# Kernel tuning notes

Hardware: AMD Instinct MI355X
Metric: run time of the kernel (lower is better)

## Reference

```python
import jax, jax.numpy as jnp
import numpy as np


def setup_inputs() -> dict:
    key = jax.random.key(0)
    k1, k2 = jax.random.split(key)
    B, M, N, D = 8, 2048, 2048, 1024
    x = jax.random.normal(k1, (B, M, D), dtype=jnp.float32)
    y = jax.random.normal(k2, (B, N, D), dtype=jnp.float32)
    return {"x": x, "y": y}


def reference(x, y):
    # scores e[b,m,n] = <x[b,m], y[b,n]>   (K.batch_dot(x, y, axes=2))
    e = jnp.einsum('bmd,bnd->bmn', x, y)
    # stable softmax over last axis (the exp/max/sum sequence in the original)
    p = jax.nn.softmax(e, axis=-1)
    # K.batch_dot(z, x, axes=1): contract axis 1 (m) of both -> [B, n, d]; V = x
    out = jnp.einsum('bmn,bmd->bnd', p, x)
    return out
```

## Files before the change

### kernel.cpp

```cpp
#include <hip/hip_runtime.h>
#include <hip/hip_bf16.h>
#include <stdint.h>

#define B_ 8
#define M_ 2048
#define N_ 2048
#define D_ 1024

typedef __bf16 bf16x8 __attribute__((ext_vector_type(8)));
typedef float f32x4 __attribute__((ext_vector_type(4)));
typedef uint16_t us4 __attribute__((ext_vector_type(4)));
typedef uint16_t us8 __attribute__((ext_vector_type(8)));

__device__ __forceinline__ uint16_t f2b(float f) {
    uint32_t u = __float_as_uint(f);
    return (uint16_t)((u + 0x7FFFu + ((u >> 16) & 1u)) >> 16);
}
__device__ __forceinline__ float b2f(uint16_t h) {
    return __uint_as_float(((uint32_t)h) << 16);
}

__device__ __forceinline__ void gld16(const uint16_t* g, const uint16_t* l) {
    __builtin_amdgcn_global_load_lds(
        (const __attribute__((address_space(1))) uint32_t*)g,
        (__attribute__((address_space(3))) uint32_t*)l,
        16, 0, 0);
}

__global__ __launch_bounds__(256) void k_split(const float* __restrict__ x,
                                               const float* __restrict__ y,
                                               uint16_t* __restrict__ xh, uint16_t* __restrict__ xl,
                                               uint16_t* __restrict__ yh, uint16_t* __restrict__ yl) {
    const int i = (blockIdx.x * 256 + threadIdx.x) * 4;
    float4 vx = *(const float4*)(x + i);
    float4 vy = *(const float4*)(y + i);
    float fx[4] = {vx.x, vx.y, vx.z, vx.w};
    float fy[4] = {vy.x, vy.y, vy.z, vy.w};
    us4 hx, lx, hy, ly;
#pragma unroll
    for (int k = 0; k < 4; ++k) {
        uint16_t h = f2b(fx[k]);
        hx[k] = h; lx[k] = f2b(fx[k] - b2f(h));
        uint16_t g = f2b(fy[k]);
        hy[k] = g; ly[k] = f2b(fy[k] - b2f(g));
    }
    *(us4*)(xh + i) = hx;
    *(us4*)(xl + i) = lx;
    *(us4*)(yh + i) = hy;
    *(us4*)(yl + i) = ly;
}

__global__ __launch_bounds__(512, 2) void k_gemm1(const uint16_t* __restrict__ xh,
                                                  const uint16_t* __restrict__ xl,
                                                  const uint16_t* __restrict__ yh,
                                                  const uint16_t* __restrict__ yl,
                                                  float* __restrict__ e,
                                                  float* __restrict__ pmax,
                                                  float* __restrict__ psum) {
    const int b = blockIdx.z;
    const int m0 = blockIdx.x * 256;
    const int n0 = blockIdx.y * 256;
    __shared__ __align__(16) uint16_t lds[65536];

    const int tid = threadIdx.x;
    const int lane = tid & 63;
    const int wid = tid >> 6;
    const int wm = (wid >> 2) * 128;
    const int wn = (wid & 3) * 64;
    const int quad = lane >> 4;
    const int r16 = lane & 15;
    const int swz8 = (quad ^ ((r16 >> 1) & 3)) * 8;

    const int base_row = wid * 16 + (lane >> 2);
    const int gd8 = ((lane & 3) ^ ((lane >> 3) & 3)) * 8;
    const uint16_t* gp[4];
    gp[0] = xh + ((size_t)b * M_ + m0 + base_row) * D_ + gd8;
    gp[1] = xl + ((size_t)b * M_ + m0 + base_row) * D_ + gd8;
    gp[2] = yh + ((size_t)b * N_ + n0 + base_row) * D_ + gd8;
    gp[3] = yl + ((size_t)b * N_ + n0 + base_row) * D_ + gd8;
    const int ldsW = wid * 512;

    const int abase = (wm + r16) * 32 + swz8;
    const int bbase = 16384 + (wn + r16) * 32 + swz8;

    f32x4 acc[8][4];
#pragma unroll
    for (int i = 0; i < 8; ++i)
#pragma unroll
        for (int j = 0; j < 4; ++j) acc[i][j] = (f32x4){0.f, 0.f, 0.f, 0.f};

    auto STAGE = [&](int dst, int ktn, int c0, int c1) {
#pragma unroll
        for (int c = c0; c < c1; ++c)
            gld16(gp[c >> 1] + (size_t)(c & 1) * (128 * D_) + ktn * 32,
                  &lds[dst + c * 4096 + ldsW]);
    };

    STAGE(0, 0, 0, 8);

    for (int kt = 0; kt < D_ / 32; ++kt) {
        const int bo = (kt & 1) << 15;
        const int nbo = bo ^ 32768;

        if (kt < D_ / 32 - 1) {
            STAGE(nbo, kt + 1, 0, 4);
            asm volatile("s_waitcnt vmcnt(4)" ::: "memory");
        } else {
            asm volatile("s_waitcnt vmcnt(0)" ::: "memory");
        }
        __builtin_amdgcn_s_barrier();
        __builtin_amdgcn_sched_barrier(0);

        bf16x8 bh[4], bl[4], ah[8], al[8];
#pragma unroll
        for (int j = 0; j < 4; ++j) {
            bh[j] = *(const bf16x8*)&lds[bo + bbase + j * 512];
            bl[j] = *(const bf16x8*)&lds[bo + bbase + 8192 + j * 512];
        }
        auto RDA = [&](int i) {
            ah[i] = *(const bf16x8*)&lds[bo + abase + i * 512];
            al[i] = *(const bf16x8*)&lds[bo + abase + 8192 + i * 512];
        };
        auto MM = [&](int i) {
#pragma unroll
            for (int j = 0; j < 4; ++j) {
                acc[i][j] = __builtin_amdgcn_mfma_f32_16x16x32_bf16(ah[i], bh[j], acc[i][j], 0, 0, 0);
                acc[i][j] = __builtin_amdgcn_mfma_f32_16x16x32_bf16(ah[i], bl[j], acc[i][j], 0, 0, 0);
                acc[i][j] = __builtin_amdgcn_mfma_f32_16x16x32_bf16(al[i], bh[j], acc[i][j], 0, 0, 0);
            }
        };

        RDA(0); RDA(1); RDA(2); RDA(3);
        __builtin_amdgcn_s_setprio(1); MM(0); MM(1); __builtin_amdgcn_s_setprio(0);
        __builtin_amdgcn_s_barrier(); __builtin_amdgcn_sched_barrier(0);
        if (kt < D_ / 32 - 1) STAGE(nbo, kt + 1, 4, 8);
        RDA(4); RDA(5);
        __builtin_amdgcn_s_setprio(1); MM(2); MM(3); __builtin_amdgcn_s_setprio(0);
        __builtin_amdgcn_s_barrier(); __builtin_amdgcn_sched_barrier(0);
        RDA(6); RDA(7);
        __builtin_amdgcn_s_setprio(1); MM(4); MM(5); __builtin_amdgcn_s_setprio(0);
        __builtin_amdgcn_s_barrier(); __builtin_amdgcn_sched_barrier(0);
        __builtin_amdgcn_s_setprio(1); MM(6); MM(7); __builtin_amdgcn_s_setprio(0);
        __builtin_amdgcn_s_barrier(); __builtin_amdgcn_sched_barrier(0);
    }

    float* eb = e + (size_t)b * M_ * N_;
    const int grows = (int)gridDim.z * M_;
    const int growbase = b * M_ + m0 + wm;
    const int nb = (n0 + wn) >> 6;
    float* pm = pmax + (size_t)nb * grows + growbase;
    float* ps = psum + (size_t)nb * grows + growbase;

#pragma unroll
    for (int i = 0; i < 8; ++i) {
#pragma unroll
        for (int r = 0; r < 4; ++r) {
            const float v0 = acc[i][0][r], v1 = acc[i][1][r];
            const float v2 = acc[i][2][r], v3 = acc[i][3][r];
            float mrow = fmaxf(fmaxf(v0, v1), fmaxf(v2, v3));
#pragma unroll
            for (int s = 1; s < 16; s <<= 1) mrow = fmaxf(mrow, __shfl_xor(mrow, s, 64));
            float srow = __expf(v0 - mrow) + __expf(v1 - mrow)
                       + __expf(v2 - mrow) + __expf(v3 - mrow);
#pragma unroll
            for (int s = 1; s < 16; s <<= 1) srow += __shfl_xor(srow, s, 64);
            const int lrow = i * 16 + quad * 4 + r;
            if (r16 == 0) { pm[lrow] = mrow; ps[lrow] = srow; }
            const size_t ebase = (size_t)(m0 + wm + lrow) * N_ + n0 + wn + r16;
#pragma unroll
            for (int j = 0; j < 4; ++j) eb[ebase + j * 16] = acc[i][j][r];
        }
    }
}

__global__ __launch_bounds__(256) void k_combine(const float* __restrict__ pmax,
                                                 const float* __restrict__ psum,
                                                 float* __restrict__ mx,
                                                 float* __restrict__ inv, int rows) {
    const int r = blockIdx.x * 256 + threadIdx.x;
    float m = -3.4e38f;
#pragma unroll
    for (int nb = 0; nb < 32; ++nb) m = fmaxf(m, pmax[(size_t)nb * rows + r]);
    float s = 0.f;
#pragma unroll
    for (int nb = 0; nb < 32; ++nb)
        s += psum[(size_t)nb * rows + r] * __expf(pmax[(size_t)nb * rows + r] - m);
    mx[r] = m;
    inv[r] = 1.0f / s;
}

__global__ __launch_bounds__(256) void k_texp(const float* __restrict__ e,
                                              const float* __restrict__ mx,
                                              const float* __restrict__ inv,
                                              uint16_t* __restrict__ pT) {
    const int b = blockIdx.z, m0 = blockIdx.x * 64, n0 = blockIdx.y * 64;
    __shared__ float tile[64 * 65];
    const int t = threadIdx.x;
    const float* eb = e + (size_t)b * M_ * N_;
#pragma unroll
    for (int q = 0; q < 4; ++q) {
        const int row = q * 16 + (t >> 4);
        const int c4 = (t & 15) * 4;
        float4 v = *(const float4*)&eb[(size_t)(m0 + row) * N_ + n0 + c4];
        const float mv = mx[b * M_ + m0 + row];
        const float iv = inv[b * M_ + m0 + row];
        tile[row * 65 + c4 + 0] = __expf(v.x - mv) * iv;
        tile[row * 65 + c4 + 1] = __expf(v.y - mv) * iv;
        tile[row * 65 + c4 + 2] = __expf(v.z - mv) * iv;
        tile[row * 65 + c4 + 3] = __expf(v.w - mv) * iv;
    }
    __syncthreads();
    uint16_t* pb = pT + (size_t)b * N_ * M_;
#pragma unroll
    for (int q = 0; q < 2; ++q) {
        const int n = q * 32 + (t >> 3);
        const int mc = (t & 7) * 8;
        us8 o;
#pragma unroll
        for (int k = 0; k < 8; ++k) o[k] = f2b(tile[(mc + k) * 65 + n]);
        *(us8*)&pb[(size_t)(n0 + n) * M_ + m0 + mc] = o;
    }
}

__global__ __launch_bounds__(256) void k_tx(const float* __restrict__ x,
                                            uint16_t* __restrict__ xt) {
    const int b = blockIdx.z, m0 = blockIdx.x * 64, d0 = blockIdx.y * 64;
    __shared__ float tile[64 * 65];
    const int t = threadIdx.x;
    const float* xb = x + (size_t)b * M_ * D_;
#pragma unroll
    for (int q = 0; q < 4; ++q) {
        const int row = q * 16 + (t >> 4);
        const int c4 = (t & 15) * 4;
        float4 v = *(const float4*)&xb[(size_t)(m0 + row) * D_ + d0 + c4];
        tile[row * 65 + c4 + 0] = v.x;
        tile[row * 65 + c4 + 1] = v.y;
        tile[row * 65 + c4 + 2] = v.z;
        tile[row * 65 + c4 + 3] = v.w;
    }
    __syncthreads();
    uint16_t* xtb = xt + (size_t)b * D_ * M_;
#pragma unroll
    for (int q = 0; q < 2; ++q) {
        const int d = q * 32 + (t >> 3);
        const int mc = (t & 7) * 8;
        us8 o;
#pragma unroll
        for (int k = 0; k < 8; ++k) o[k] = f2b(tile[(mc + k) * 65 + d]);
        *(us8*)&xtb[(size_t)(d0 + d) * M_ + m0 + mc] = o;
    }
}

__global__ __launch_bounds__(256) void k_gemm2(const uint16_t* __restrict__ pT,
                                               const uint16_t* __restrict__ xt,
                                               float* __restrict__ out) {
    const int b = blockIdx.z;
    const int n0 = blockIdx.x * 128;
    const int d0 = blockIdx.y * 128;
    __shared__ __align__(16) uint16_t lds[16384];

    const int tid = threadIdx.x;
    const int lane = tid & 63;
    const int wid = tid >> 6;
    const int wn = (wid & 1) * 64;
    const int wd = (wid >> 1) * 64;
    const int quad = lane >> 4;
    const int r16 = lane & 15;

    const uint16_t* srcA = pT + ((size_t)b * N_ + n0) * M_;
    const uint16_t* srcB = xt + ((size_t)b * D_ + d0) * M_;

    f32x4 acc[4][4];
#pragma unroll
    for (int i = 0; i < 4; ++i)
#pragma unroll
        for (int j = 0; j < 4; ++j) acc[i][j] = (f32x4){0.f, 0.f, 0.f, 0.f};

    for (int kt = 0; kt < M_ / 64; ++kt) {
#pragma unroll
        for (int c = 0; c < 8; ++c) {
            const int offbase = c * 2048 + wid * 512;
            const int tile = offbase >> 13;
            const int o = (offbase & 8191) + lane * 8;
            const int row = o >> 6;
            const int gp = (o & 63) >> 3;
            const int gd = gp ^ (row & 7);
            const uint16_t* sp = tile ? srcB : srcA;
            gld16(sp + (size_t)row * M_ + kt * 64 + gd * 8, &lds[offbase]);
        }
        __syncthreads();

#pragma unroll
        for (int h = 0; h < 2; ++h) {
            const int p = (h * 4 + quad) ^ (r16 & 7);
            bf16x8 a[4], bb[4];
#pragma unroll
            for (int i = 0; i < 4; ++i) {
                a[i]  = *(const bf16x8*)&lds[(wn + i * 16 + r16) * 64 + p * 8];
                bb[i] = *(const bf16x8*)&lds[8192 + (wd + i * 16 + r16) * 64 + p * 8];
            }
#pragma unroll
            for (int i = 0; i < 4; ++i)
#pragma unroll
                for (int j = 0; j < 4; ++j)
                    acc[i][j] = __builtin_amdgcn_mfma_f32_16x16x32_bf16(a[i], bb[j], acc[i][j], 0, 0, 0);
        }
        __syncthreads();
    }

    float* ob = out + (size_t)b * N_ * D_;
#pragma unroll
    for (int i = 0; i < 4; ++i) {
        const int rbase = n0 + wn + i * 16 + quad * 4;
#pragma unroll
        for (int j = 0; j < 4; ++j) {
            const int col = d0 + wd + j * 16 + r16;
#pragma unroll
            for (int r = 0; r < 4; ++r)
                ob[(size_t)(rbase + r) * D_ + col] = acc[i][j][r];
        }
    }
}

extern "C" void kernel_launch(void* const* d_in, const int* in_sizes, int n_in,
                              void* d_out, int out_size, void* d_ws, size_t ws_size,
                              hipStream_t stream) {
    const float* x = (const float*)d_in[0];
    const float* y = (const float*)d_in[1];
    float* out = (float*)d_out;
    char* ws = (char*)d_ws;

    const size_t MiB = 1024 * 1024;
    int g = 8;
    while (g > 1 && (size_t)g * 32 * MiB > ws_size) g >>= 1;
    if ((size_t)g * 32 * MiB > ws_size) return;

    const size_t T = (size_t)g * M_ * D_ * 2;
    uint16_t* xh = (uint16_t*)(ws + 0 * T);
    uint16_t* xl = (uint16_t*)(ws + 1 * T);
    uint16_t* yh = (uint16_t*)(ws + 2 * T);
    uint16_t* yl = (uint16_t*)(ws + 3 * T);
    float*    e  = (float*)(ws + 4 * T);
    float*    mx = (float*)(ws);
    float*    inv = mx + (size_t)g * M_;
    uint16_t* xt = xl;
    uint16_t* pT = yh;

    const size_t pelems = (size_t)32 * g * M_;
    float* pmax = (float*)d_out + (size_t)B_ * N_ * D_ - 2 * pelems;
    float* psum = pmax + pelems;

    for (int c0 = 0; c0 < B_; c0 += g) {
        const float* xc = x + (size_t)c0 * M_ * D_;
        const float* yc = y + (size_t)c0 * N_ * D_;
        float* oc = out + (size_t)c0 * N_ * D_;

        hipLaunchKernelGGL(k_split, dim3((g * M_ * D_) / (256 * 4)), dim3(256), 0, stream,
                           xc, yc, xh, xl, yh, yl);
        hipLaunchKernelGGL(k_gemm1, dim3(M_ / 256, N_ / 256, g), dim3(512), 0, stream,
                           xh, xl, yh, yl, e, pmax, psum);
        hipLaunchKernelGGL(k_combine, dim3((g * M_) / 256), dim3(256), 0, stream,
                           pmax, psum, mx, inv, g * M_);
        hipLaunchKernelGGL(k_texp, dim3(M_ / 64, N_ / 64, g), dim3(256), 0, stream,
                           e, mx, inv, pT);
        hipLaunchKernelGGL(k_tx, dim3(M_ / 64, D_ / 64, g), dim3(256), 0, stream, xc, xt);
        hipLaunchKernelGGL(k_gemm2, dim3(N_ / 128, D_ / 128, g), dim3(256), 0, stream,
                           pT, xt, oc);
    }
}
```

Baseline: 507.4 us.

## Restructure split-bf16 GEMM1 as a K-extended GEMM with interleaved staging

The score GEMM no longer issues three MFMAs per k-step over hi/lo pairs. It now treats the computation as one longer K loop of 3×1024 that walks the (xh,yh), (xh,yl) and (xl,yh) segments with 64-wide k tiles. LDS tiles change to 64-column swizzled rows, the A and B buffers are double-buffered on separate schedules, and global-to-LDS loads are spread across four MFMA phases with barriers between them. The aim is fewer register-resident fragments and better overlap of loads with MFMA work, at the cost of more barriers and harder-to-follow buffer indexing.

```diff
diff --git a/kernel.cpp b/kernel.cpp
--- a/kernel.cpp
+++ b/kernel.cpp
@@ -49,6 +49,28 @@
     *(us4*)(yh + i) = hy;
     *(us4*)(yl + i) = ly;
 }
+
+#define BAR1 do { __builtin_amdgcn_sched_barrier(0); __builtin_amdgcn_s_barrier(); \
+                  __builtin_amdgcn_sched_barrier(0); } while (0)
+#define LD8(off) (*(const bf16x8*)&lds[off])
+#define RDA(bo32, q)                                                   \
+    a[0][0] = LD8((bo32) + aoff + ((q)*2) * 1024 + e0);                \
+    a[0][1] = LD8((bo32) + aoff + ((q)*2) * 1024 + e1);                \
+    a[1][0] = LD8((bo32) + aoff + ((q)*2 + 1) * 1024 + e0);            \
+    a[1][1] = LD8((bo32) + aoff + ((q)*2 + 1) * 1024 + e1);
+#define RDB(bo32)                                                      \
+    _Pragma("unroll") for (int j = 0; j < 4; ++j) {                    \
+        bb[j][0] = LD8((bo32) + boff + j * 1024 + e0);                 \
+        bb[j][1] = LD8((bo32) + boff + j * 1024 + e1);                 \
+    }
+#define MFMA16(q)                                                      \
+    __builtin_amdgcn_s_setprio(1);                                     \
+    _Pragma("unroll") for (int kh = 0; kh < 2; ++kh)                   \
+    _Pragma("unroll") for (int ii = 0; ii < 2; ++ii)                   \
+    _Pragma("unroll") for (int j = 0; j < 4; ++j)                      \
+        acc[(q)*2 + ii][j] = __builtin_amdgcn_mfma_f32_16x16x32_bf16(  \
+            a[ii][kh], bb[j][kh], acc[(q)*2 + ii][j], 0, 0, 0);        \
+    __builtin_amdgcn_s_setprio(0);
 
 __global__ __launch_bounds__(512, 2) void k_gemm1(const uint16_t* __restrict__ xh,
                                                   const uint16_t* __restrict__ xl,
@@ -69,19 +91,25 @@
     const int wn = (wid & 3) * 64;
     const int quad = lane >> 4;
     const int r16 = lane & 15;
-    const int swz8 = (quad ^ ((r16 >> 1) & 3)) * 8;
-
-    const int base_row = wid * 16 + (lane >> 2);
-    const int gd8 = ((lane & 3) ^ ((lane >> 3) & 3)) * 8;
-    const uint16_t* gp[4];
-    gp[0] = xh + ((size_t)b * M_ + m0 + base_row) * D_ + gd8;
-    gp[1] = xl + ((size_t)b * M_ + m0 + base_row) * D_ + gd8;
-    gp[2] = yh + ((size_t)b * N_ + n0 + base_row) * D_ + gd8;
-    gp[3] = yl + ((size_t)b * N_ + n0 + base_row) * D_ + gd8;
-    const int ldsW = wid * 512;
-
-    const int abase = (wm + r16) * 32 + swz8;
-    const int bbase = 16384 + (wn + r16) * 32 + swz8;
+    const int rb7 = r16 & 7;
+    const int e0 = (quad ^ rb7) * 8;
+    const int e1 = ((quad + 4) ^ rb7) * 8;
+    const int aoff = (wm + r16) * 64;
+    const int boff = 16384 + (wn + r16) * 64;
+
+    const int srow = tid >> 3;
+    const int gd8 = ((tid & 7) ^ ((tid >> 3) & 7)) * 8;
+
+    auto Ab = [&](int kt) {
+        return (kt < 32 ? xh : xl) + ((size_t)b * M_ + m0) * D_ + (kt & 15) * 64 + gd8;
+    };
+    auto Bb = [&](int kt) {
+        return (((kt >> 4) == 1) ? yl : yh) + ((size_t)b * N_ + n0) * D_ + (kt & 15) * 64 + gd8;
+    };
+    auto SH = [&](int dst, const uint16_t* srcb, int h) {
+        gld16(srcb + (size_t)(h * 128 + srow) * D_, &lds[dst + h * 8192 + wid * 512]);
+        gld16(srcb + (size_t)(h * 128 + 64 + srow) * D_, &lds[dst + h * 8192 + 4096 + wid * 512]);
+    };
 
     f32x4 acc[8][4];
 #pragma unroll
@@ -89,59 +117,57 @@
 #pragma unroll
         for (int j = 0; j < 4; ++j) acc[i][j] = (f32x4){0.f, 0.f, 0.f, 0.f};
 
-    auto STAGE = [&](int dst, int ktn, int c0, int c1) {
-#pragma unroll
-        for (int c = c0; c < c1; ++c)
-            gld16(gp[c >> 1] + (size_t)(c & 1) * (128 * D_) + ktn * 32,
-                  &lds[dst + c * 4096 + ldsW]);
-    };
-
-    STAGE(0, 0, 0, 8);
-
-    for (int kt = 0; kt < D_ / 32; ++kt) {
-        const int bo = (kt & 1) << 15;
-        const int nbo = bo ^ 32768;
-
-        if (kt < D_ / 32 - 1) {
-            STAGE(nbo, kt + 1, 0, 4);
-            asm volatile("s_waitcnt vmcnt(4)" ::: "memory");
-        } else {
-            asm volatile("s_waitcnt vmcnt(0)" ::: "memory");
-        }
-        __builtin_amdgcn_s_barrier();
-        __builtin_amdgcn_sched_barrier(0);
-
-        bf16x8 bh[4], bl[4], ah[8], al[8];
-#pragma unroll
-        for (int j = 0; j < 4; ++j) {
-            bh[j] = *(const bf16x8*)&lds[bo + bbase + j * 512];
-            bl[j] = *(const bf16x8*)&lds[bo + bbase + 8192 + j * 512];
-        }
-        auto RDA = [&](int i) {
-            ah[i] = *(const bf16x8*)&lds[bo + abase + i * 512];
-            al[i] = *(const bf16x8*)&lds[bo + abase + 8192 + i * 512];
-        };
-        auto MM = [&](int i) {
-#pragma unroll
-            for (int j = 0; j < 4; ++j) {
-                acc[i][j] = __builtin_amdgcn_mfma_f32_16x16x32_bf16(ah[i], bh[j], acc[i][j], 0, 0, 0);
-                acc[i][j] = __builtin_amdgcn_mfma_f32_16x16x32_bf16(ah[i], bl[j], acc[i][j], 0, 0, 0);
-                acc[i][j] = __builtin_amdgcn_mfma_f32_16x16x32_bf16(al[i], bh[j], acc[i][j], 0, 0, 0);
-            }
-        };
-
-        RDA(0); RDA(1); RDA(2); RDA(3);
-        __builtin_amdgcn_s_setprio(1); MM(0); MM(1); __builtin_amdgcn_s_setprio(0);
-        __builtin_amdgcn_s_barrier(); __builtin_amdgcn_sched_barrier(0);
-        if (kt < D_ / 32 - 1) STAGE(nbo, kt + 1, 4, 8);
-        RDA(4); RDA(5);
-        __builtin_amdgcn_s_setprio(1); MM(2); MM(3); __builtin_amdgcn_s_setprio(0);
-        __builtin_amdgcn_s_barrier(); __builtin_amdgcn_sched_barrier(0);
-        RDA(6); RDA(7);
-        __builtin_amdgcn_s_setprio(1); MM(4); MM(5); __builtin_amdgcn_s_setprio(0);
-        __builtin_amdgcn_s_barrier(); __builtin_amdgcn_sched_barrier(0);
-        __builtin_amdgcn_s_setprio(1); MM(6); MM(7); __builtin_amdgcn_s_setprio(0);
-        __builtin_amdgcn_s_barrier(); __builtin_amdgcn_sched_barrier(0);
+    bf16x8 a[2][2], bb[4][2];
+
+    SH(0, Ab(0), 0); SH(0, Ab(0), 1);
+    SH(16384, Bb(0), 0); SH(16384, Bb(0), 1);
+    SH(49152, Bb(1), 0); SH(49152, Bb(1), 1);
+    asm volatile("s_waitcnt vmcnt(4)" ::: "memory");
+    __builtin_amdgcn_s_barrier();
+    __builtin_amdgcn_sched_barrier(0);
+
+    for (int t = 0; t < 24; ++t) {
+        const bool s2 = t < 23;
+        const uint16_t* a1p = Ab(2 * t + 1);
+        const uint16_t* a2p = Ab(2 * t + 2);
+        const uint16_t* b2p = Bb(2 * t + 2);
+        const uint16_t* b3p = Bb(2 * t + 3);
+
+        RDB(0); RDA(0, 0);
+        SH(32768, a1p, 0);
+        BAR1; MFMA16(0); BAR1;
+
+        RDA(0, 1);
+        SH(32768, a1p, 1);
+        if (s2) SH(16384, b2p, 0);
+        BAR1; MFMA16(1); BAR1;
+
+        RDA(0, 2);
+        if (s2) SH(16384, b2p, 1);
+        BAR1; MFMA16(2); BAR1;
+
+        RDA(0, 3);
+        BAR1; MFMA16(3);
+        if (s2) { asm volatile("s_waitcnt vmcnt(4)" ::: "memory"); }
+        else    { asm volatile("s_waitcnt vmcnt(0)" ::: "memory"); }
+        BAR1;
+
+        RDB(32768); RDA(32768, 0);
+        if (s2) SH(0, a2p, 0);
+        BAR1; MFMA16(0); BAR1;
+
+        RDA(32768, 1);
+        if (s2) { SH(0, a2p, 1); SH(49152, b3p, 0); }
+        BAR1; MFMA16(1); BAR1;
+
+        RDA(32768, 2);
+        if (s2) SH(49152, b3p, 1);
+        BAR1; MFMA16(2); BAR1;
+
+        RDA(32768, 3);
+        BAR1; MFMA16(3);
+        if (s2) { asm volatile("s_waitcnt vmcnt(4)" ::: "memory"); }
+        BAR1;
     }
 
     float* eb = e + (size_t)b * M_ * N_;
@@ -160,12 +186,12 @@
             float mrow = fmaxf(fmaxf(v0, v1), fmaxf(v2, v3));
 #pragma unroll
             for (int s = 1; s < 16; s <<= 1) mrow = fmaxf(mrow, __shfl_xor(mrow, s, 64));
-            float srow = __expf(v0 - mrow) + __expf(v1 - mrow)
-                       + __expf(v2 - mrow) + __expf(v3 - mrow);
-#pragma unroll
-            for (int s = 1; s < 16; s <<= 1) srow += __shfl_xor(srow, s, 64);
+            float srow_ = __expf(v0 - mrow) + __expf(v1 - mrow)
+                        + __expf(v2 - mrow) + __expf(v3 - mrow);
+#pragma unroll
+            for (int s = 1; s < 16; s <<= 1) srow_ += __shfl_xor(srow_, s, 64);
             const int lrow = i * 16 + quad * 4 + r;
-            if (r16 == 0) { pm[lrow] = mrow; ps[lrow] = srow; }
+            if (r16 == 0) { pm[lrow] = mrow; ps[lrow] = srow_; }
             const size_t ebase = (size_t)(m0 + wm + lrow) * N_ + n0 + wn + r16;
 #pragma unroll
             for (int j = 0; j < 4; ++j) eb[ebase + j * 16] = acc[i][j][r];
@@ -293,17 +319,17 @@
 #pragma unroll
         for (int h = 0; h < 2; ++h) {
             const int p = (h * 4 + quad) ^ (r16 & 7);
-            bf16x8 a[4], bb[4];
+            bf16x8 a[4], bbr[4];
 #pragma unroll
             for (int i = 0; i < 4; ++i) {
-                a[i]  = *(const bf16x8*)&lds[(wn + i * 16 + r16) * 64 + p * 8];
-                bb[i] = *(const bf16x8*)&lds[8192 + (wd + i * 16 + r16) * 64 + p * 8];
+                a[i]   = *(const bf16x8*)&lds[(wn + i * 16 + r16) * 64 + p * 8];
+                bbr[i] = *(const bf16x8*)&lds[8192 + (wd + i * 16 + r16) * 64 + p * 8];
             }
 #pragma unroll
             for (int i = 0; i < 4; ++i)
 #pragma unroll
                 for (int j = 0; j < 4; ++j)
-                    acc[i][j] = __builtin_amdgcn_mfma_f32_16x16x32_bf16(a[i], bb[j], acc[i][j], 0, 0, 0);
+                    acc[i][j] = __builtin_amdgcn_mfma_f32_16x16x32_bf16(a[i], bbr[j], acc[i][j], 0, 0, 0);
         }
         __syncthreads();
     }
```

After: 515.0 us. About the same (+1.5%).

## Software-pipeline LDS fragment reads in gemm1 with ping-pong A registers

Applied to the files above, without the earlier changes.

Restructures the k_gemm1 main loop so the A fragments for the next quarter are read from LDS while MFMAs for the current quarter run, using two ping-pong register sets. The next K-tile's first A and B fragments are prefetched before the loop iteration ends. The number of workgroup barriers per tile drops from five to two, and the global-to-LDS stage is issued as one batch of eight loads. This hides LDS latency behind matrix work and cuts barrier stalls, but it waits on all outstanding global loads (vmcnt(0)) mid-iteration, which may expose global latency, and it raises register pressure. Variable renames elsewhere are cosmetic.

```diff
diff --git a/kernel.cpp b/kernel.cpp
--- a/kernel.cpp
+++ b/kernel.cpp
@@ -49,6 +49,31 @@
     *(us4*)(yh + i) = hy;
     *(us4*)(yl + i) = ly;
 }
+
+#define SBAR0 __builtin_amdgcn_sched_barrier(0)
+#define LD8(off) (*(const bf16x8*)&lds[off])
+#define RDB(bo)                                                        \
+    _Pragma("unroll") for (int j = 0; j < 4; ++j) {                    \
+        bh[j] = LD8((bo) + bbase + j * 512);                           \
+        bl[j] = LD8((bo) + bbase + 8192 + j * 512);                    \
+    }
+#define RDA(H, L, bo, q)                                               \
+    H[0] = LD8((bo) + abase + ((q)*2) * 512);                          \
+    H[1] = LD8((bo) + abase + ((q)*2 + 1) * 512);                      \
+    L[0] = LD8((bo) + abase + 8192 + ((q)*2) * 512);                   \
+    L[1] = LD8((bo) + abase + 8192 + ((q)*2 + 1) * 512);
+#define MMQ(H, L, q)                                                   \
+    __builtin_amdgcn_s_setprio(1);                                     \
+    _Pragma("unroll") for (int ii = 0; ii < 2; ++ii)                   \
+    _Pragma("unroll") for (int j = 0; j < 4; ++j) {                    \
+        acc[(q)*2 + ii][j] = __builtin_amdgcn_mfma_f32_16x16x32_bf16(  \
+            H[ii], bh[j], acc[(q)*2 + ii][j], 0, 0, 0);                \
+        acc[(q)*2 + ii][j] = __builtin_amdgcn_mfma_f32_16x16x32_bf16(  \
+            H[ii], bl[j], acc[(q)*2 + ii][j], 0, 0, 0);                \
+        acc[(q)*2 + ii][j] = __builtin_amdgcn_mfma_f32_16x16x32_bf16(  \
+            L[ii], bh[j], acc[(q)*2 + ii][j], 0, 0, 0);                \
+    }                                                                  \
+    __builtin_amdgcn_s_setprio(0);
 
 __global__ __launch_bounds__(512, 2) void k_gemm1(const uint16_t* __restrict__ xh,
                                                   const uint16_t* __restrict__ xl,
@@ -83,65 +108,60 @@
     const int abase = (wm + r16) * 32 + swz8;
     const int bbase = 16384 + (wn + r16) * 32 + swz8;
 
-    f32x4 acc[8][4];
-#pragma unroll
-    for (int i = 0; i < 8; ++i)
-#pragma unroll
-        for (int j = 0; j < 4; ++j) acc[i][j] = (f32x4){0.f, 0.f, 0.f, 0.f};
-
-    auto STAGE = [&](int dst, int ktn, int c0, int c1) {
-#pragma unroll
-        for (int c = c0; c < c1; ++c)
+    auto STAGE = [&](int dst, int ktn) {
+#pragma unroll
+        for (int c = 0; c < 8; ++c)
             gld16(gp[c >> 1] + (size_t)(c & 1) * (128 * D_) + ktn * 32,
                   &lds[dst + c * 4096 + ldsW]);
     };
 
-    STAGE(0, 0, 0, 8);
-
-    for (int kt = 0; kt < D_ / 32; ++kt) {
-        const int bo = (kt & 1) << 15;
+    f32x4 acc[8][4];
+#pragma unroll
+    for (int i = 0; i < 8; ++i)
+#pragma unroll
+        for (int j = 0; j < 4; ++j) acc[i][j] = (f32x4){0.f, 0.f, 0.f, 0.f};
+
+    bf16x8 bh[4], bl[4];
+    bf16x8 a0h[2], a0l[2];
+    bf16x8 a1h[2], a1l[2];
+
+    STAGE(0, 0);
+    asm volatile("s_waitcnt vmcnt(0)" ::: "memory");
+    SBAR0; __builtin_amdgcn_s_barrier(); SBAR0;
+    RDB(0); RDA(a0h, a0l, 0, 0);
+
+    for (int t = 0; t < 32; ++t) {
+        const int bo = (t & 1) << 15;
         const int nbo = bo ^ 32768;
-
-        if (kt < D_ / 32 - 1) {
-            STAGE(nbo, kt + 1, 0, 4);
-            asm volatile("s_waitcnt vmcnt(4)" ::: "memory");
-        } else {
-            asm volatile("s_waitcnt vmcnt(0)" ::: "memory");
-        }
-        __builtin_amdgcn_s_barrier();
-        __builtin_amdgcn_sched_barrier(0);
-
-        bf16x8 bh[4], bl[4], ah[8], al[8];
-#pragma unroll
-        for (int j = 0; j < 4; ++j) {
-            bh[j] = *(const bf16x8*)&lds[bo + bbase + j * 512];
-            bl[j] = *(const bf16x8*)&lds[bo + bbase + 8192 + j * 512];
-        }
-        auto RDA = [&](int i) {
-            ah[i] = *(const bf16x8*)&lds[bo + abase + i * 512];
-            al[i] = *(const bf16x8*)&lds[bo + abase + 8192 + i * 512];
-        };
-        auto MM = [&](int i) {
-#pragma unroll
-            for (int j = 0; j < 4; ++j) {
-                acc[i][j] = __builtin_amdgcn_mfma_f32_16x16x32_bf16(ah[i], bh[j], acc[i][j], 0, 0, 0);
-                acc[i][j] = __builtin_amdgcn_mfma_f32_16x16x32_bf16(ah[i], bl[j], acc[i][j], 0, 0, 0);
-                acc[i][j] = __builtin_amdgcn_mfma_f32_16x16x32_bf16(al[i], bh[j], acc[i][j], 0, 0, 0);
-            }
-        };
-
-        RDA(0); RDA(1); RDA(2); RDA(3);
-        __builtin_amdgcn_s_setprio(1); MM(0); MM(1); __builtin_amdgcn_s_setprio(0);
-        __builtin_amdgcn_s_barrier(); __builtin_amdgcn_sched_barrier(0);
-        if (kt < D_ / 32 - 1) STAGE(nbo, kt + 1, 4, 8);
-        RDA(4); RDA(5);
-        __builtin_amdgcn_s_setprio(1); MM(2); MM(3); __builtin_amdgcn_s_setprio(0);
-        __builtin_amdgcn_s_barrier(); __builtin_amdgcn_sched_barrier(0);
-        RDA(6); RDA(7);
-        __builtin_amdgcn_s_setprio(1); MM(4); MM(5); __builtin_amdgcn_s_setprio(0);
-        __builtin_amdgcn_s_barrier(); __builtin_amdgcn_sched_barrier(0);
-        __builtin_amdgcn_s_setprio(1); MM(6); MM(7); __builtin_amdgcn_s_setprio(0);
-        __builtin_amdgcn_s_barrier(); __builtin_amdgcn_sched_barrier(0);
+        const bool more = t < 31;
+
+        if (more) STAGE(nbo, t + 1);
+        RDA(a1h, a1l, bo, 1);
+        SBAR0;
+        MMQ(a0h, a0l, 0);
+        SBAR0;
+
+        RDA(a0h, a0l, bo, 2);
+        SBAR0;
+        MMQ(a1h, a1l, 1);
+        SBAR0;
+
+        RDA(a1h, a1l, bo, 3);
+        SBAR0;
+        MMQ(a0h, a0l, 2);
+        SBAR0;
+
+        asm volatile("s_waitcnt vmcnt(0)" ::: "memory");
+        SBAR0; __builtin_amdgcn_s_barrier(); SBAR0;
+
+        if (more) { RDA(a0h, a0l, nbo, 0); }
+        SBAR0;
+        MMQ(a1h, a1l, 3);
+        SBAR0;
+        if (more) {
+            RDB(nbo);
+            SBAR0; __builtin_amdgcn_s_barrier(); SBAR0;
+        }
     }
 
     float* eb = e + (size_t)b * M_ * N_;
@@ -160,12 +180,12 @@
             float mrow = fmaxf(fmaxf(v0, v1), fmaxf(v2, v3));
 #pragma unroll
             for (int s = 1; s < 16; s <<= 1) mrow = fmaxf(mrow, __shfl_xor(mrow, s, 64));
-            float srow = __expf(v0 - mrow) + __expf(v1 - mrow)
-                       + __expf(v2 - mrow) + __expf(v3 - mrow);
-#pragma unroll
-            for (int s = 1; s < 16; s <<= 1) srow += __shfl_xor(srow, s, 64);
+            float srow_ = __expf(v0 - mrow) + __expf(v1 - mrow)
+                        + __expf(v2 - mrow) + __expf(v3 - mrow);
+#pragma unroll
+            for (int s = 1; s < 16; s <<= 1) srow_ += __shfl_xor(srow_, s, 64);
             const int lrow = i * 16 + quad * 4 + r;
-            if (r16 == 0) { pm[lrow] = mrow; ps[lrow] = srow; }
+            if (r16 == 0) { pm[lrow] = mrow; ps[lrow] = srow_; }
             const size_t ebase = (size_t)(m0 + wm + lrow) * N_ + n0 + wn + r16;
 #pragma unroll
             for (int j = 0; j < 4; ++j) eb[ebase + j * 16] = acc[i][j][r];
@@ -293,17 +313,17 @@
 #pragma unroll
         for (int h = 0; h < 2; ++h) {
             const int p = (h * 4 + quad) ^ (r16 & 7);
-            bf16x8 a[4], bb[4];
+            bf16x8 a[4], bbr[4];
 #pragma unroll
             for (int i = 0; i < 4; ++i) {
-                a[i]  = *(const bf16x8*)&lds[(wn + i * 16 + r16) * 64 + p * 8];
-                bb[i] = *(const bf16x8*)&lds[8192 + (wd + i * 16 + r16) * 64 + p * 8];
+                a[i]   = *(const bf16x8*)&lds[(wn + i * 16 + r16) * 64 + p * 8];
+                bbr[i] = *(const bf16x8*)&lds[8192 + (wd + i * 16 + r16) * 64 + p * 8];
             }
 #pragma unroll
             for (int i = 0; i < 4; ++i)
 #pragma unroll
                 for (int j = 0; j < 4; ++j)
-                    acc[i][j] = __builtin_amdgcn_mfma_f32_16x16x32_bf16(a[i], bb[j], acc[i][j], 0, 0, 0);
+                    acc[i][j] = __builtin_amdgcn_mfma_f32_16x16x32_bf16(a[i], bbr[j], acc[i][j], 0, 0, 0);
         }
         __syncthreads();
     }
```

Result: no change. 498.9 us (-1.7%).

## Shrink gemm1 tiles to 128x128 and double-buffer gemm2 LDS

Applied to the files above, without the earlier changes.

The score GEMM now uses 128x128 tiles with 8 waves of 64x32 each, less LDS and an occupancy hint of 4. Its hand-tuned split staging, setprio and barrier schedule is replaced by plain double buffering with __syncthreads, and partial softmax stats now span 64 column blocks. The second GEMM gains a double-buffered LDS pipeline that prefetches the next K tile while computing the current one. Smaller tiles give each wave fewer MFMAs per LDS load, so global and LDS traffic per flop go up, and the hand-made overlap in gemm1 is lost.

```diff
diff --git a/kernel.cpp b/kernel.cpp
--- a/kernel.cpp
+++ b/kernel.cpp
@@ -50,7 +50,7 @@
     *(us4*)(yl + i) = ly;
 }
 
-__global__ __launch_bounds__(512, 2) void k_gemm1(const uint16_t* __restrict__ xh,
+__global__ __launch_bounds__(512, 4) void k_gemm1(const uint16_t* __restrict__ xh,
                                                   const uint16_t* __restrict__ xl,
                                                   const uint16_t* __restrict__ yh,
                                                   const uint16_t* __restrict__ yl,
@@ -58,117 +58,96 @@
                                                   float* __restrict__ pmax,
                                                   float* __restrict__ psum) {
     const int b = blockIdx.z;
-    const int m0 = blockIdx.x * 256;
-    const int n0 = blockIdx.y * 256;
-    __shared__ __align__(16) uint16_t lds[65536];
+    const int m0 = blockIdx.x * 128;
+    const int n0 = blockIdx.y * 128;
+    __shared__ __align__(16) uint16_t lds[32768];
 
     const int tid = threadIdx.x;
     const int lane = tid & 63;
     const int wid = tid >> 6;
-    const int wm = (wid >> 2) * 128;
-    const int wn = (wid & 3) * 64;
+    const int wm = (wid >> 2) * 64;
+    const int wn = (wid & 3) * 32;
     const int quad = lane >> 4;
     const int r16 = lane & 15;
     const int swz8 = (quad ^ ((r16 >> 1) & 3)) * 8;
 
-    const int base_row = wid * 16 + (lane >> 2);
-    const int gd8 = ((lane & 3) ^ ((lane >> 3) & 3)) * 8;
-    const uint16_t* gp[4];
-    gp[0] = xh + ((size_t)b * M_ + m0 + base_row) * D_ + gd8;
-    gp[1] = xl + ((size_t)b * M_ + m0 + base_row) * D_ + gd8;
-    gp[2] = yh + ((size_t)b * N_ + n0 + base_row) * D_ + gd8;
-    gp[3] = yl + ((size_t)b * N_ + n0 + base_row) * D_ + gd8;
+    const int row0 = wid * 16 + (lane >> 2);
+    const int gd8 = ((lane & 3) ^ ((row0 >> 1) & 3)) * 8;
+    const uint16_t* sp[4];
+    sp[0] = xh + ((size_t)b * M_ + m0 + row0) * D_ + gd8;
+    sp[1] = xl + ((size_t)b * M_ + m0 + row0) * D_ + gd8;
+    sp[2] = yh + ((size_t)b * N_ + n0 + row0) * D_ + gd8;
+    sp[3] = yl + ((size_t)b * N_ + n0 + row0) * D_ + gd8;
     const int ldsW = wid * 512;
 
+    auto STAGE = [&](int dst, int ktn) {
+#pragma unroll
+        for (int c = 0; c < 4; ++c)
+            gld16(sp[c] + ktn * 32, &lds[dst + c * 4096 + ldsW]);
+    };
+
     const int abase = (wm + r16) * 32 + swz8;
-    const int bbase = 16384 + (wn + r16) * 32 + swz8;
-
-    f32x4 acc[8][4];
-#pragma unroll
-    for (int i = 0; i < 8; ++i)
-#pragma unroll
-        for (int j = 0; j < 4; ++j) acc[i][j] = (f32x4){0.f, 0.f, 0.f, 0.f};
-
-    auto STAGE = [&](int dst, int ktn, int c0, int c1) {
-#pragma unroll
-        for (int c = c0; c < c1; ++c)
-            gld16(gp[c >> 1] + (size_t)(c & 1) * (128 * D_) + ktn * 32,
-                  &lds[dst + c * 4096 + ldsW]);
-    };
-
-    STAGE(0, 0, 0, 8);
+    const int bbase = 8192 + (wn + r16) * 32 + swz8;
+
+    f32x4 acc[4][2];
+#pragma unroll
+    for (int i = 0; i < 4; ++i)
+#pragma unroll
+        for (int j = 0; j < 2; ++j) acc[i][j] = (f32x4){0.f, 0.f, 0.f, 0.f};
+
+    STAGE(0, 0);
+    __syncthreads();
 
     for (int kt = 0; kt < D_ / 32; ++kt) {
-        const int bo = (kt & 1) << 15;
-        const int nbo = bo ^ 32768;
-
-        if (kt < D_ / 32 - 1) {
-            STAGE(nbo, kt + 1, 0, 4);
-            asm volatile("s_waitcnt vmcnt(4)" ::: "memory");
-        } else {
-            asm volatile("s_waitcnt vmcnt(0)" ::: "memory");
-        }
-        __builtin_amdgcn_s_barrier();
-        __builtin_amdgcn_sched_barrier(0);
-
-        bf16x8 bh[4], bl[4], ah[8], al[8];
-#pragma unroll
-        for (int j = 0; j < 4; ++j) {
+        const int bo = (kt & 1) << 14;
+        const int nbo = bo ^ 16384;
+        if (kt < D_ / 32 - 1) STAGE(nbo, kt + 1);
+
+        bf16x8 ah[4], al[4], bh[2], bl[2];
+#pragma unroll
+        for (int j = 0; j < 2; ++j) {
             bh[j] = *(const bf16x8*)&lds[bo + bbase + j * 512];
-            bl[j] = *(const bf16x8*)&lds[bo + bbase + 8192 + j * 512];
-        }
-        auto RDA = [&](int i) {
+            bl[j] = *(const bf16x8*)&lds[bo + bbase + 4096 + j * 512];
+        }
+#pragma unroll
+        for (int i = 0; i < 4; ++i) {
             ah[i] = *(const bf16x8*)&lds[bo + abase + i * 512];
-            al[i] = *(const bf16x8*)&lds[bo + abase + 8192 + i * 512];
-        };
-        auto MM = [&](int i) {
-#pragma unroll
-            for (int j = 0; j < 4; ++j) {
+            al[i] = *(const bf16x8*)&lds[bo + abase + 4096 + i * 512];
+        }
+#pragma unroll
+        for (int i = 0; i < 4; ++i)
+#pragma unroll
+            for (int j = 0; j < 2; ++j) {
                 acc[i][j] = __builtin_amdgcn_mfma_f32_16x16x32_bf16(ah[i], bh[j], acc[i][j], 0, 0, 0);
                 acc[i][j] = __builtin_amdgcn_mfma_f32_16x16x32_bf16(ah[i], bl[j], acc[i][j], 0, 0, 0);
                 acc[i][j] = __builtin_amdgcn_mfma_f32_16x16x32_bf16(al[i], bh[j], acc[i][j], 0, 0, 0);
             }
-        };
-
-        RDA(0); RDA(1); RDA(2); RDA(3);
-        __builtin_amdgcn_s_setprio(1); MM(0); MM(1); __builtin_amdgcn_s_setprio(0);
-        __builtin_amdgcn_s_barrier(); __builtin_amdgcn_sched_barrier(0);
-        if (kt < D_ / 32 - 1) STAGE(nbo, kt + 1, 4, 8);
-        RDA(4); RDA(5);
-        __builtin_amdgcn_s_setprio(1); MM(2); MM(3); __builtin_amdgcn_s_setprio(0);
-        __builtin_amdgcn_s_barrier(); __builtin_amdgcn_sched_barrier(0);
-        RDA(6); RDA(7);
-        __builtin_amdgcn_s_setprio(1); MM(4); MM(5); __builtin_amdgcn_s_setprio(0);
-        __builtin_amdgcn_s_barrier(); __builtin_amdgcn_sched_barrier(0);
-        __builtin_amdgcn_s_setprio(1); MM(6); MM(7); __builtin_amdgcn_s_setprio(0);
-        __builtin_amdgcn_s_barrier(); __builtin_amdgcn_sched_barrier(0);
+        __syncthreads();
     }
 
     float* eb = e + (size_t)b * M_ * N_;
     const int grows = (int)gridDim.z * M_;
     const int growbase = b * M_ + m0 + wm;
-    const int nb = (n0 + wn) >> 6;
+    const int nb = (n0 + wn) >> 5;
     float* pm = pmax + (size_t)nb * grows + growbase;
     float* ps = psum + (size_t)nb * grows + growbase;
 
 #pragma unroll
-    for (int i = 0; i < 8; ++i) {
+    for (int i = 0; i < 4; ++i) {
 #pragma unroll
         for (int r = 0; r < 4; ++r) {
             const float v0 = acc[i][0][r], v1 = acc[i][1][r];
-            const float v2 = acc[i][2][r], v3 = acc[i][3][r];
-            float mrow = fmaxf(fmaxf(v0, v1), fmaxf(v2, v3));
+            float mrow = fmaxf(v0, v1);
 #pragma unroll
             for (int s = 1; s < 16; s <<= 1) mrow = fmaxf(mrow, __shfl_xor(mrow, s, 64));
-            float srow = __expf(v0 - mrow) + __expf(v1 - mrow)
-                       + __expf(v2 - mrow) + __expf(v3 - mrow);
-#pragma unroll
-            for (int s = 1; s < 16; s <<= 1) srow += __shfl_xor(srow, s, 64);
+            float srow_ = __expf(v0 - mrow) + __expf(v1 - mrow);
+#pragma unroll
+            for (int s = 1; s < 16; s <<= 1) srow_ += __shfl_xor(srow_, s, 64);
             const int lrow = i * 16 + quad * 4 + r;
-            if (r16 == 0) { pm[lrow] = mrow; ps[lrow] = srow; }
+            if (r16 == 0) { pm[lrow] = mrow; ps[lrow] = srow_; }
             const size_t ebase = (size_t)(m0 + wm + lrow) * N_ + n0 + wn + r16;
 #pragma unroll
-            for (int j = 0; j < 4; ++j) eb[ebase + j * 16] = acc[i][j][r];
+            for (int j = 0; j < 2; ++j) eb[ebase + j * 16] = acc[i][j][r];
         }
     }
 }
@@ -180,10 +159,10 @@
     const int r = blockIdx.x * 256 + threadIdx.x;
     float m = -3.4e38f;
 #pragma unroll
-    for (int nb = 0; nb < 32; ++nb) m = fmaxf(m, pmax[(size_t)nb * rows + r]);
+    for (int nb = 0; nb < 64; ++nb) m = fmaxf(m, pmax[(size_t)nb * rows + r]);
     float s = 0.f;
 #pragma unroll
-    for (int nb = 0; nb < 32; ++nb)
+    for (int nb = 0; nb < 64; ++nb)
         s += psum[(size_t)nb * rows + r] * __expf(pmax[(size_t)nb * rows + r] - m);
     mx[r] = m;
     inv[r] = 1.0f / s;
@@ -257,7 +236,7 @@
     const int b = blockIdx.z;
     const int n0 = blockIdx.x * 128;
     const int d0 = blockIdx.y * 128;
-    __shared__ __align__(16) uint16_t lds[16384];
+    __shared__ __align__(16) uint16_t lds[32768];
 
     const int tid = threadIdx.x;
     const int lane = tid & 63;
@@ -276,7 +255,7 @@
 #pragma unroll
         for (int j = 0; j < 4; ++j) acc[i][j] = (f32x4){0.f, 0.f, 0.f, 0.f};
 
-    for (int kt = 0; kt < M_ / 64; ++kt) {
+    auto STAGE = [&](int dst, int kt) {
 #pragma unroll
         for (int c = 0; c < 8; ++c) {
             const int offbase = c * 2048 + wid * 512;
@@ -286,24 +265,32 @@
             const int gp = (o & 63) >> 3;
             const int gd = gp ^ (row & 7);
             const uint16_t* sp = tile ? srcB : srcA;
-            gld16(sp + (size_t)row * M_ + kt * 64 + gd * 8, &lds[offbase]);
-        }
-        __syncthreads();
+            gld16(sp + (size_t)row * M_ + kt * 64 + gd * 8, &lds[dst + offbase]);
+        }
+    };
+
+    STAGE(0, 0);
+    __syncthreads();
+
+    for (int kt = 0; kt < M_ / 64; ++kt) {
+        const int bo = (kt & 1) << 14;
+        const int nbo = bo ^ 16384;
+        if (kt < M_ / 64 - 1) STAGE(nbo, kt + 1);
 
 #pragma unroll
         for (int h = 0; h < 2; ++h) {
             const int p = (h * 4 + quad) ^ (r16 & 7);
-            bf16x8 a[4], bb[4];
+            bf16x8 a[4], bbr[4];
 #pragma unroll
             for (int i = 0; i < 4; ++i) {
-                a[i]  = *(const bf16x8*)&lds[(wn + i * 16 + r16) * 64 + p * 8];
-                bb[i] = *(const bf16x8*)&lds[8192 + (wd + i * 16 + r16) * 64 + p * 8];
+                a[i]   = *(const bf16x8*)&lds[bo + (wn + i * 16 + r16) * 64 + p * 8];
+                bbr[i] = *(const bf16x8*)&lds[bo + 8192 + (wd + i * 16 + r16) * 64 + p * 8];
             }
 #pragma unroll
             for (int i = 0; i < 4; ++i)
 #pragma unroll
                 for (int j = 0; j < 4; ++j)
-                    acc[i][j] = __builtin_amdgcn_mfma_f32_16x16x32_bf16(a[i], bb[j], acc[i][j], 0, 0, 0);
+                    acc[i][j] = __builtin_amdgcn_mfma_f32_16x16x32_bf16(a[i], bbr[j], acc[i][j], 0, 0, 0);
         }
         __syncthreads();
     }
@@ -346,7 +333,7 @@
     uint16_t* xt = xl;
     uint16_t* pT = yh;
 
-    const size_t pelems = (size_t)32 * g * M_;
+    const size_t pelems = (size_t)64 * g * M_;
     float* pmax = (float*)d_out + (size_t)B_ * N_ * D_ - 2 * pelems;
     float* psum = pmax + pelems;
 
@@ -357,7 +344,7 @@
 
         hipLaunchKernelGGL(k_split, dim3((g * M_ * D_) / (256 * 4)), dim3(256), 0, stream,
                            xc, yc, xh, xl, yh, yl);
-        hipLaunchKernelGGL(k_gemm1, dim3(M_ / 256, N_ / 256, g), dim3(512), 0, stream,
+        hipLaunchKernelGGL(k_gemm1, dim3(M_ / 128, N_ / 128, g), dim3(512), 0, stream,
                            xh, xl, yh, yl, e, pmax, psum);
         hipLaunchKernelGGL(k_combine, dim3((g * M_) / 256), dim3(256), 0, stream,
                            pmax, psum, mx, inv, g * M_);
```

New measurement: 520.5 us. 1.03x slower.
